# Kernel tuning notes

Hardware: AMD Instinct MI355X
Metric: run time of the kernel (lower is better)

Reference implementation:

```python
import jax, jax.numpy as jnp
import numpy as np

MOMENTUM = 0.2   # cfg.CAP.MOMENTUM
TEMP = 0.05      # cfg.CAP.TEMP
N_BANK = 131072  # number of instance rows in the memory bank
D_FEAT = 1024    # feature dim
BATCH = 64


def _l2_normalize(x, axis=-1, eps=1e-12):
    return x / jnp.maximum(jnp.linalg.norm(x, axis=axis, keepdims=True), eps)


def setup_inputs() -> dict:
    key = jax.random.key(0)
    k1, k2, k3 = jax.random.split(key, 3)
    inputs = jax.random.normal(k1, (BATCH, D_FEAT), dtype=jnp.float32)
    features = jax.random.normal(k2, (N_BANK, D_FEAT), dtype=jnp.float32)
    # bank rows are kept unit-norm by the renorm step of the module
    features = _l2_normalize(features, axis=1)
    indexes = jax.random.randint(k3, (BATCH,), 0, N_BANK)
    return {"inputs": inputs, "indexes": indexes, "features": features}


def reference(inputs, indexes, features):
    # --- forward of InstanceMemory/CameraMemory.apply ---
    # cfg.CAP.NORM_FEAT: L2-normalize the batch features first
    x = _l2_normalize(inputs, axis=1)                 # [B, D]
    # mm lookup against the memory bank, scaled by temperature
    sim = (x @ features.T) / TEMP                      # [B, N]

    # --- per-sample sequential momentum scatter update + renorm ---
    # original: for x, y in zip(inputs, indexes):
    #   features[y] = m*features[y] + (1-m)*x; features[y] /= ||features[y]||
    # sequential semantics matter when indexes repeat -> lax.scan recurrence
    def step(feats, xy):
        xi, yi = xy
        row = feats[yi]                                # [D] gather
        new = MOMENTUM * row + (1.0 - MOMENTUM) * xi
        new = new / jnp.maximum(jnp.linalg.norm(new), 1e-12)
        return feats.at[yi].set(new), None             # [D] scatter

    new_features, _ = jax.lax.scan(step, features, (x, indexes))
    return sim, new_features
```

## Files before the change

kernel.cpp:

```cpp
#include <hip/hip_runtime.h>
#include <hip/hip_bf16.h>

#define NBANK 131072
#define DF 1024
#define NB 64

typedef float f32x4 __attribute__((ext_vector_type(4)));
typedef short bf16x8 __attribute__((ext_vector_type(8)));

__device__ __forceinline__ unsigned short f2bf(float f) {
    union { float f; unsigned u; } c; c.f = f;
    unsigned u = c.u;
    return (unsigned short)((u + 0x7FFFu + ((u >> 16) & 1u)) >> 16);
}

__global__ __launch_bounds__(128) void knorm(const float* __restrict__ inputs,
                                             float* __restrict__ x_f32,
                                             bf16x8* __restrict__ xfrag) {
    int m = blockIdx.x;
    int t = threadIdx.x;
    const f32x4* row = (const f32x4*)(inputs + (size_t)m * DF);
    f32x4 v0 = row[t * 2];
    f32x4 v1 = row[t * 2 + 1];
    float s = v0.x*v0.x + v0.y*v0.y + v0.z*v0.z + v0.w*v0.w
            + v1.x*v1.x + v1.y*v1.y + v1.z*v1.z + v1.w*v1.w;
    for (int o = 32; o > 0; o >>= 1) s += __shfl_xor(s, o);
    __shared__ float red[2];
    if ((t & 63) == 0) red[t >> 6] = s;
    __syncthreads();
    float tot = red[0] + red[1];
    float inv = 1.0f / fmaxf(sqrtf(tot), 1e-12f);
    v0 *= inv; v1 *= inv;
    f32x4* xr = (f32x4*)(x_f32 + (size_t)m * DF);
    xr[t * 2]     = v0;
    xr[t * 2 + 1] = v1;
    unsigned short h[8] = { f2bf(v0.x), f2bf(v0.y), f2bf(v0.z), f2bf(v0.w),
                            f2bf(v1.x), f2bf(v1.y), f2bf(v1.z), f2bf(v1.w) };
    int idx = ((m >> 4) * 32 + (t >> 2)) * 64 + (t & 3) * 16 + (m & 15);
    xfrag[idx] = *(bf16x8*)h;
}

__global__ __launch_bounds__(256) void kmain(const float* __restrict__ features,
                                             const bf16x8* __restrict__ xfrag,
                                             const int* __restrict__ indexes,
                                             const float* __restrict__ x_f32,
                                             float* __restrict__ sim,
                                             float* __restrict__ outf) {
    __shared__ __align__(16) unsigned char tile[16 * 2048];
    __shared__ float red[4];
    int j0 = blockIdx.x * 16;
    int t = threadIdx.x;

    unsigned urmask = 0;
#pragma unroll 8
    for (int j = 0; j < NB; ++j) {
        unsigned d = (unsigned)(indexes[j] - j0);
        if (d < 16u) urmask |= (1u << d);
    }

    f32x4 v[16];
#pragma unroll
    for (int p = 0; p < 16; ++p)
        v[p] = *((const f32x4*)(features + (size_t)(j0 + p) * DF) + t);
#pragma unroll
    for (int p = 0; p < 16; ++p) {
        __builtin_nontemporal_store(v[p], (f32x4*)(outf + (size_t)(j0 + p) * DF) + t);
        unsigned lo = (unsigned)f2bf(v[p].x) | ((unsigned)f2bf(v[p].y) << 16);
        unsigned hi = (unsigned)f2bf(v[p].z) | ((unsigned)f2bf(v[p].w) << 16);
        uint2 pk; pk.x = lo; pk.y = hi;
        unsigned off = (unsigned)(p * 2048) + (((unsigned)(t * 8)) ^ ((unsigned)(p & 7) << 4));
        *(uint2*)(tile + off) = pk;
    }
    __syncthreads();

    int wave = t >> 6;
    int lane = t & 63;
    const bf16x8* af = xfrag + (size_t)(wave * 32) * 64 + lane;
    unsigned brow = lane & 15;
    unsigned bbase = brow * 2048;
    unsigned bswz = (brow & 7) << 4;
    unsigned bcol = (unsigned)(lane >> 4) * 16;
    f32x4 acc = {0.f, 0.f, 0.f, 0.f};
#pragma unroll 8
    for (int ks = 0; ks < 32; ++ks) {
        bf16x8 a = af[ks * 64];
        bf16x8 b = *(const bf16x8*)(tile + bbase + (((unsigned)(ks * 64) + bcol) ^ bswz));
        acc = __builtin_amdgcn_mfma_f32_16x16x32_bf16(a, b, acc, 0, 0, 0);
    }
    int m0 = wave * 16 + (lane >> 4) * 4;
    int n = j0 + (lane & 15);
#pragma unroll
    for (int r = 0; r < 4; ++r)
        __builtin_nontemporal_store(acc[r] * 20.0f,
                                    sim + (size_t)(m0 + r) * NBANK + n);

    if (urmask) {
        for (int p = 0; p < 16; ++p) {
            if (!((urmask >> p) & 1)) continue;
            int row = j0 + p;
            f32x4 cur = *((const f32x4*)(features + (size_t)row * DF) + t);
            for (int j = 0; j < NB; ++j) {
                if (indexes[j] != row) continue;
                f32x4 xv = *((const f32x4*)(x_f32 + (size_t)j * DF) + t);
                cur = cur * 0.2f + xv * 0.8f;
                float s = cur.x*cur.x + cur.y*cur.y + cur.z*cur.z + cur.w*cur.w;
                for (int o = 32; o > 0; o >>= 1) s += __shfl_xor(s, o);
                if ((t & 63) == 0) red[t >> 6] = s;
                __syncthreads();
                float tot = red[0] + red[1] + red[2] + red[3];
                __syncthreads();
                float inv = 1.0f / fmaxf(sqrtf(tot), 1e-12f);
                cur *= inv;
            }
            *((f32x4*)(outf + (size_t)row * DF) + t) = cur;
        }
    }
}

extern "C" void kernel_launch(void* const* d_in, const int* in_sizes, int n_in,
                              void* d_out, int out_size, void* d_ws, size_t ws_size,
                              hipStream_t stream) {
    const float* inputs   = (const float*)d_in[0];
    const int*   indexes  = (const int*)d_in[1];
    const float* features = (const float*)d_in[2];
    float* sim  = (float*)d_out;
    float* outf = sim + (size_t)NB * NBANK;
    float*  x_f32 = (float*)d_ws;
    bf16x8* xfrag = (bf16x8*)((char*)d_ws + (size_t)NB * DF * 4);

    knorm<<<NB, 128, 0, stream>>>(inputs, x_f32, xfrag);
    kmain<<<NBANK / 16, 256, 0, stream>>>(features, xfrag, indexes, x_f32, sim, outf);
}
```

Measured before the change: 230.3 us.

## Make kmain persistent with register-cached A fragments and prefetched feature tiles

The main kernel becomes persistent: a fixed grid of 1024 blocks loops over 8 tiles each. The x bf16 fragments are loaded into registers once per block, and the next tile's features are prefetched into registers while the current tile's MFMA and sim stores run. The per-tile update masks are now precomputed in the normalize kernel instead of every block scanning the indexes. This removes per-block launch and A-fragment reload overhead and overlaps HBM reads with compute, at the cost of heavy register pressure (32 bf16x8 plus 16 f32x4 per thread) under a 5-waves occupancy hint, which may cause spills.

```diff
diff --git a/kernel.cpp b/kernel.cpp
--- a/kernel.cpp
+++ b/kernel.cpp
@@ -4,6 +4,9 @@
 #define NBANK 131072
 #define DF 1024
 #define NB 64
+#define NT (NBANK / 16)
+#define GRID 1024
+#define TPB (NT / GRID)
 
 typedef float f32x4 __attribute__((ext_vector_type(4)));
 typedef short bf16x8 __attribute__((ext_vector_type(8)));
@@ -15,17 +18,21 @@
 }
 
 __global__ __launch_bounds__(128) void knorm(const float* __restrict__ inputs,
+                                             const int* __restrict__ indexes,
                                              float* __restrict__ x_f32,
-                                             bf16x8* __restrict__ xfrag) {
+                                             bf16x8* __restrict__ xfrag,
+                                             unsigned* __restrict__ urs) {
     int m = blockIdx.x;
     int t = threadIdx.x;
+    __shared__ float red[2];
+    __shared__ int sidx[NB];
+    if (t < NB) sidx[t] = indexes[t];
     const f32x4* row = (const f32x4*)(inputs + (size_t)m * DF);
     f32x4 v0 = row[t * 2];
     f32x4 v1 = row[t * 2 + 1];
     float s = v0.x*v0.x + v0.y*v0.y + v0.z*v0.z + v0.w*v0.w
             + v1.x*v1.x + v1.y*v1.y + v1.z*v1.z + v1.w*v1.w;
     for (int o = 32; o > 0; o >>= 1) s += __shfl_xor(s, o);
-    __shared__ float red[2];
     if ((t & 63) == 0) red[t >> 6] = s;
     __syncthreads();
     float tot = red[0] + red[1];
@@ -38,82 +45,98 @@
                             f2bf(v1.x), f2bf(v1.y), f2bf(v1.z), f2bf(v1.w) };
     int idx = ((m >> 4) * 32 + (t >> 2)) * 64 + (t & 3) * 16 + (m & 15);
     xfrag[idx] = *(bf16x8*)h;
+    int tile = m * 128 + t;
+    int j0 = tile * 16;
+    unsigned mask = 0;
+#pragma unroll 8
+    for (int j = 0; j < NB; ++j) {
+        unsigned d = (unsigned)(sidx[j] - j0);
+        if (d < 16u) mask |= (1u << d);
+    }
+    urs[tile] = mask;
 }
 
-__global__ __launch_bounds__(256) void kmain(const float* __restrict__ features,
-                                             const bf16x8* __restrict__ xfrag,
-                                             const int* __restrict__ indexes,
-                                             const float* __restrict__ x_f32,
-                                             float* __restrict__ sim,
-                                             float* __restrict__ outf) {
-    __shared__ __align__(16) unsigned char tile[16 * 2048];
-    __shared__ float red[4];
-    int j0 = blockIdx.x * 16;
+__global__ __launch_bounds__(256, 5) void kmain(const float* __restrict__ features,
+                                                const bf16x8* __restrict__ xfrag,
+                                                const int* __restrict__ indexes,
+                                                const float* __restrict__ x_f32,
+                                                const unsigned* __restrict__ urs,
+                                                float* __restrict__ sim,
+                                                float* __restrict__ outf) {
+    __shared__ __align__(16) unsigned char tile[32768];
     int t = threadIdx.x;
+    int wave = t >> 6;
+    int lane = t & 63;
 
-    unsigned urmask = 0;
-#pragma unroll 8
-    for (int j = 0; j < NB; ++j) {
-        unsigned d = (unsigned)(indexes[j] - j0);
-        if (d < 16u) urmask |= (1u << d);
-    }
+    bf16x8 af[32];
+#pragma unroll
+    for (int ks = 0; ks < 32; ++ks)
+        af[ks] = xfrag[(size_t)(wave * 32 + ks) * 64 + lane];
 
+    unsigned bbase = (unsigned)(lane & 15) * 2048;
+    unsigned bswz  = (unsigned)(lane & 7) << 4;
+    unsigned bcol  = (unsigned)(lane >> 4) * 16;
+    int m0 = wave * 16 + (lane >> 4) * 4;
+
+    int tileIdx = blockIdx.x;
     f32x4 v[16];
 #pragma unroll
     for (int p = 0; p < 16; ++p)
-        v[p] = *((const f32x4*)(features + (size_t)(j0 + p) * DF) + t);
+        v[p] = *((const f32x4*)(features + (size_t)(tileIdx * 16 + p) * DF) + t);
+
+    for (int it = 0; it < TPB; ++it) {
+        int j0 = tileIdx * 16;
+        unsigned urmask = urs[tileIdx];
 #pragma unroll
-    for (int p = 0; p < 16; ++p) {
-        __builtin_nontemporal_store(v[p], (f32x4*)(outf + (size_t)(j0 + p) * DF) + t);
-        unsigned lo = (unsigned)f2bf(v[p].x) | ((unsigned)f2bf(v[p].y) << 16);
-        unsigned hi = (unsigned)f2bf(v[p].z) | ((unsigned)f2bf(v[p].w) << 16);
-        uint2 pk; pk.x = lo; pk.y = hi;
-        unsigned off = (unsigned)(p * 2048) + (((unsigned)(t * 8)) ^ ((unsigned)(p & 7) << 4));
-        *(uint2*)(tile + off) = pk;
-    }
-    __syncthreads();
-
-    int wave = t >> 6;
-    int lane = t & 63;
-    const bf16x8* af = xfrag + (size_t)(wave * 32) * 64 + lane;
-    unsigned brow = lane & 15;
-    unsigned bbase = brow * 2048;
-    unsigned bswz = (brow & 7) << 4;
-    unsigned bcol = (unsigned)(lane >> 4) * 16;
-    f32x4 acc = {0.f, 0.f, 0.f, 0.f};
-#pragma unroll 8
-    for (int ks = 0; ks < 32; ++ks) {
-        bf16x8 a = af[ks * 64];
-        bf16x8 b = *(const bf16x8*)(tile + bbase + (((unsigned)(ks * 64) + bcol) ^ bswz));
-        acc = __builtin_amdgcn_mfma_f32_16x16x32_bf16(a, b, acc, 0, 0, 0);
-    }
-    int m0 = wave * 16 + (lane >> 4) * 4;
-    int n = j0 + (lane & 15);
+        for (int p = 0; p < 16; ++p) {
+            __builtin_nontemporal_store(v[p], (f32x4*)(outf + (size_t)(j0 + p) * DF) + t);
+            unsigned lo = (unsigned)f2bf(v[p].x) | ((unsigned)f2bf(v[p].y) << 16);
+            unsigned hi = (unsigned)f2bf(v[p].z) | ((unsigned)f2bf(v[p].w) << 16);
+            uint2 pk; pk.x = lo; pk.y = hi;
+            unsigned off = (unsigned)(p * 2048) + (((unsigned)(t * 8)) ^ ((unsigned)(p & 7) << 4));
+            *(uint2*)(tile + off) = pk;
+        }
+        asm volatile("s_waitcnt lgkmcnt(0)\n\ts_barrier" ::: "memory");
+        int nextIdx = tileIdx + GRID;
+        if (it + 1 < TPB) {
 #pragma unroll
-    for (int r = 0; r < 4; ++r)
-        __builtin_nontemporal_store(acc[r] * 20.0f,
-                                    sim + (size_t)(m0 + r) * NBANK + n);
-
-    if (urmask) {
-        for (int p = 0; p < 16; ++p) {
-            if (!((urmask >> p) & 1)) continue;
-            int row = j0 + p;
-            f32x4 cur = *((const f32x4*)(features + (size_t)row * DF) + t);
-            for (int j = 0; j < NB; ++j) {
-                if (indexes[j] != row) continue;
-                f32x4 xv = *((const f32x4*)(x_f32 + (size_t)j * DF) + t);
-                cur = cur * 0.2f + xv * 0.8f;
-                float s = cur.x*cur.x + cur.y*cur.y + cur.z*cur.z + cur.w*cur.w;
-                for (int o = 32; o > 0; o >>= 1) s += __shfl_xor(s, o);
-                if ((t & 63) == 0) red[t >> 6] = s;
-                __syncthreads();
-                float tot = red[0] + red[1] + red[2] + red[3];
-                __syncthreads();
-                float inv = 1.0f / fmaxf(sqrtf(tot), 1e-12f);
-                cur *= inv;
+            for (int p = 0; p < 16; ++p)
+                v[p] = *((const f32x4*)(features + (size_t)(nextIdx * 16 + p) * DF) + t);
+        }
+        f32x4 acc = {0.f, 0.f, 0.f, 0.f};
+#pragma unroll
+        for (int ks = 0; ks < 32; ++ks) {
+            bf16x8 b = *(const bf16x8*)(tile + bbase + (((unsigned)(ks * 64) + bcol) ^ bswz));
+            acc = __builtin_amdgcn_mfma_f32_16x16x32_bf16(af[ks], b, acc, 0, 0, 0);
+        }
+#pragma unroll
+        for (int r = 0; r < 4; ++r)
+            __builtin_nontemporal_store(acc[r] * 20.0f,
+                sim + (size_t)(m0 + r) * NBANK + j0 + (lane & 15));
+        asm volatile("s_barrier" ::: "memory");
+        if (urmask) {
+            float* red = (float*)tile;
+            for (int p = 0; p < 16; ++p) {
+                if (!((urmask >> p) & 1)) continue;
+                int row = j0 + p;
+                f32x4 cur = *((const f32x4*)(features + (size_t)row * DF) + t);
+                for (int j = 0; j < NB; ++j) {
+                    if (indexes[j] != row) continue;
+                    f32x4 xv = *((const f32x4*)(x_f32 + (size_t)j * DF) + t);
+                    cur = cur * 0.2f + xv * 0.8f;
+                    float s = cur.x*cur.x + cur.y*cur.y + cur.z*cur.z + cur.w*cur.w;
+                    for (int o = 32; o > 0; o >>= 1) s += __shfl_xor(s, o);
+                    if ((t & 63) == 0) red[t >> 6] = s;
+                    __syncthreads();
+                    float tot = red[0] + red[1] + red[2] + red[3];
+                    __syncthreads();
+                    float inv = 1.0f / fmaxf(sqrtf(tot), 1e-12f);
+                    cur *= inv;
+                }
+                *((f32x4*)(outf + (size_t)row * DF) + t) = cur;
             }
-            *((f32x4*)(outf + (size_t)row * DF) + t) = cur;
         }
+        tileIdx = nextIdx;
     }
 }
 
@@ -125,9 +148,10 @@
     const float* features = (const float*)d_in[2];
     float* sim  = (float*)d_out;
     float* outf = sim + (size_t)NB * NBANK;
-    float*  x_f32 = (float*)d_ws;
-    bf16x8* xfrag = (bf16x8*)((char*)d_ws + (size_t)NB * DF * 4);
+    float*    x_f32 = (float*)d_ws;
+    bf16x8*   xfrag = (bf16x8*)((char*)d_ws + (size_t)NB * DF * 4);
+    unsigned* urs   = (unsigned*)((char*)d_ws + (size_t)NB * DF * 6);
 
-    knorm<<<NB, 128, 0, stream>>>(inputs, x_f32, xfrag);
-    kmain<<<NBANK / 16, 256, 0, stream>>>(features, xfrag, indexes, x_f32, sim, outf);
+    knorm<<<NB, 128, 0, stream>>>(inputs, indexes, x_f32, xfrag, urs);
+    kmain<<<GRID, 256, 0, stream>>>(features, xfrag, indexes, x_f32, urs, sim, outf);
 }
```

New measurement: 399.0 us. 73.2% more time.
